# Optimization experiments

Hardware: AMD Instinct MI355X
Metric: run time of the kernel (lower is better)

## Reference

```python
import jax, jax.numpy as jnp
import numpy as np

N = 4096          # nodes in DAG
K = 14            # parents per non-root node
C = 1 << K        # CPT configurations per node
N_ROOTS = 64      # nodes with no parents
EPS = 1e-6


def setup_inputs() -> dict:
    key = jax.random.key(0)
    # CPT logits: original init is log(p/(1-p)) with p~U[0.1,0.9] -> roughly N(0,1)-scale
    logits = jax.random.normal(key, (N, C), dtype=jnp.float32)
    # DAG structure: node i >= N_ROOTS has K parents drawn from [0, i) => identity order is topological
    rng = np.random.default_rng(0)
    parents = np.zeros((N, K), dtype=np.int32)
    for i in range(N_ROOTS, N):
        parents[i] = rng.integers(0, i, size=K)
    root_mask = np.arange(N) < N_ROOTS
    # binary configuration matrix, MSB-first, same as _configs_matrix
    ints = np.arange(C)
    configs = ((ints[:, None] >> np.arange(K - 1, -1, -1)) & 1).astype(np.float32)  # [C, K]
    return {
        "logits": logits,
        "configs": jnp.asarray(configs),
        "parents": jnp.asarray(parents),
        "root_mask": jnp.asarray(root_mask),
    }


def reference(logits, configs, parents, root_mask):
    min_val = jnp.log(jnp.float32(EPS))
    max_val = jnp.log(jnp.float32(1.0 - EPS))

    def step(log_marg, xs):
        idx, logit_row, par, is_root = xs
        log_p_cpt = jax.nn.log_sigmoid(logit_row)                    # [C]
        plp = jnp.clip(log_marg[par], min_val, max_val)              # [K] parent log-marginals
        log1m = jnp.log1p(-jnp.minimum(jnp.exp(plp), 1.0 - EPS))     # [K] log(1 - p_parent)
        # sum_k configs*plp + (1-configs)*log1m == configs @ (plp - log1m) + sum(log1m)
        log_prod = configs @ (plp - log1m) + jnp.sum(log1m)          # [C]
        lm_nonroot = jax.nn.logsumexp(log_prod + log_p_cpt)
        lm = jnp.where(is_root, log_p_cpt[0], lm_nonroot)
        return log_marg.at[idx].set(lm), None

    n = logits.shape[0]
    init = jnp.zeros((n,), dtype=jnp.float32)
    xs = (jnp.arange(n), logits, parents, root_mask)
    log_marginals, _ = jax.lax.scan(step, init, xs)
    return jnp.exp(log_marginals)
```

## Files before the change

kernel.cpp:

```cpp
#include <hip/hip_runtime.h>
#include <math.h>
#include <stdint.h>


#define NN     4096
#define KK     14
#define CC     16384
#define NROOTS 64
#define NBLK   256
#define NTHR   1024
#define PT     (CC / NTHR)
#define SENTIN 0x7F7F7F7Fu

__global__ __launch_bounds__(NTHR, 4) void bayes_dag_kernel(
    const float* __restrict__ logits,
    const int*   __restrict__ parents,
    float*       __restrict__ out,
    unsigned*    __restrict__ flagv)
{
    __shared__ float pvals[KK];
    __shared__ float redLds[NTHR / 64];

    const int tid  = threadIdx.x;
    const int lane = tid & 63;
    const int wv   = tid >> 6;
    const float LOG2E = 1.4426950408889634f;

    int node = blockIdx.x;
    if (node < NROOTS) {
        if (tid == 0) {
            float x = logits[(size_t)node * CC];
            float p = __builtin_amdgcn_rcpf(1.f + exp2f(-x * LOG2E));
            out[node] = p;
            __hip_atomic_store(&flagv[node], __float_as_uint(p),
                               __ATOMIC_RELAXED, __HIP_MEMORY_SCOPE_AGENT);
        }
        node += NBLK;
    }

    float xs[PT];
    {
        const float* row = logits + (size_t)node * CC;
        #pragma unroll
        for (int m = 0; m < PT; ++m) xs[m] = row[m * NTHR + tid];
    }

    for (; node < NN; node += NBLK) {
        const int   nxt  = node + NBLK;
        const float* nrow = logits + (size_t)(nxt < NN ? nxt : node) * CC;
        float xn[PT];
        #pragma unroll
        for (int m = 0; m < PT; ++m) xn[m] = nrow[m * NTHR + tid];

        float sig[PT];
        #pragma unroll
        for (int m = 0; m < PT; ++m)
            sig[m] = __builtin_amdgcn_rcpf(1.f + exp2f(-xs[m] * LOG2E));

        if (wv == 0) {
            int p = 0;
            if (lane < KK) p = parents[node * KK + lane];
            unsigned v = SENTIN;
            int guard = 0;
            for (;;) {
                if (lane < KK)
                    v = __hip_atomic_load(&flagv[p], __ATOMIC_RELAXED,
                                          __HIP_MEMORY_SCOPE_AGENT);
                if (__all(lane >= KK || v != SENTIN)) break;
                if (++guard > (1 << 22)) break;
                __builtin_amdgcn_s_sleep(1);
            }
            if (lane < KK) {
                float pf = __uint_as_float(v);
                pvals[lane] = fminf(fmaxf(pf, 1e-6f), 1.f - 1e-6f);
            }
        }
        __syncthreads();

        float pv[KK];
        #pragma unroll
        for (int k = 0; k < KK; ++k) pv[k] = pvals[k];

        float v8[8];
        #pragma unroll
        for (int j = 0; j < 8; ++j)
            v8[j] = fmaf(pv[3], sig[2*j+1] - sig[2*j], sig[2*j]);
        float v4[4];
        #pragma unroll
        for (int j = 0; j < 4; ++j)
            v4[j] = fmaf(pv[2], v8[2*j+1] - v8[2*j], v8[2*j]);
        float v2[2];
        #pragma unroll
        for (int j = 0; j < 2; ++j)
            v2[j] = fmaf(pv[1], v4[2*j+1] - v4[2*j], v4[2*j]);
        float acc = fmaf(pv[0], v2[1] - v2[0], v2[0]);

        #pragma unroll
        for (int t = 0; t < 6; ++t) {
            float other = __shfl_xor(acc, 1 << t, 64);
            bool  bit   = (lane >> t) & 1;
            float a = bit ? other : acc;
            float b = bit ? acc : other;
            acc = fmaf(pv[13 - t], b - a, a);
        }
        if (lane == 0) redLds[wv] = acc;
        __syncthreads();

        if (wv == 0) {
            float val = (lane < NTHR / 64) ? redLds[lane] : 0.f;
            #pragma unroll
            for (int t = 0; t < 4; ++t) {
                float other = __shfl_xor(val, 1 << t, 64);
                bool  bit   = (lane >> t) & 1;
                float a = bit ? other : val;
                float b = bit ? val : other;
                val = fmaf(pv[7 - t], b - a, a);
            }
            if (lane == 0) {
                out[node] = val;
                __hip_atomic_store(&flagv[node], __float_as_uint(val),
                                   __ATOMIC_RELAXED, __HIP_MEMORY_SCOPE_AGENT);
            }
        }

        #pragma unroll
        for (int m = 0; m < PT; ++m) xs[m] = xn[m];
    }
}

extern "C" void kernel_launch(void* const* d_in, const int* in_sizes, int n_in,
                              void* d_out, int out_size, void* d_ws, size_t ws_size,
                              hipStream_t stream) {
    const float* logits  = (const float*)d_in[0];
    const int*   parents = (const int*)d_in[2];
    float*    out   = (float*)d_out;
    unsigned* flagv = (unsigned*)d_ws;

    hipMemsetAsync(flagv, 0x7F, NN * sizeof(unsigned), stream);

    void* args[] = { (void*)&logits, (void*)&parents, (void*)&out, (void*)&flagv };
    hipLaunchCooperativeKernel((const void*)bayes_dag_kernel,
                               dim3(NBLK), dim3(NTHR), args, 0, stream);
}
```

Measured before the change: 623.3 us.

## Start reduction with one missing parent and defer its fold to the end

The parent-wait loop now exits once all but one parent marginal is available. The block reduces the CPT tensor over every other parent, keeping two partial results split on the missing parent's bit, and waits for that last parent only just before the final fold. Next-node parent indices are prefetched, and the sleep in the poll loop is removed. This is meant to shorten the critical dependency chain across blocks, at the cost of more complex branching, duplicated shuffle reductions and busier polling.

```diff
diff --git a/kernel.cpp b/kernel.cpp
--- a/kernel.cpp
+++ b/kernel.cpp
@@ -12,6 +12,11 @@
 #define PT     (CC / NTHR)
 #define SENTIN 0x7F7F7F7Fu
 
+#define FOLD2(p, x0, x1) fmaf((p), (x1) - (x0), (x0))
+#define FOLD8(pA, pB, pC, s0,s1,s2,s3,s4,s5,s6,s7) \
+    FOLD2(pC, FOLD2(pB, FOLD2(pA, s0, s1), FOLD2(pA, s2, s3)), \
+              FOLD2(pB, FOLD2(pA, s4, s5), FOLD2(pA, s6, s7)))
+
 __global__ __launch_bounds__(NTHR, 4) void bayes_dag_kernel(
     const float* __restrict__ logits,
     const int*   __restrict__ parents,
@@ -19,7 +24,10 @@
     unsigned*    __restrict__ flagv)
 {
     __shared__ float pvals[KK];
-    __shared__ float redLds[NTHR / 64];
+    __shared__ int   sSlotLds;
+    __shared__ int   sParLds;
+    __shared__ float redA[NTHR / 64];
+    __shared__ float redB[NTHR / 64];
 
     const int tid  = threadIdx.x;
     const int lane = tid & 63;
@@ -31,9 +39,9 @@
         if (tid == 0) {
             float x = logits[(size_t)node * CC];
             float p = __builtin_amdgcn_rcpf(1.f + exp2f(-x * LOG2E));
-            out[node] = p;
             __hip_atomic_store(&flagv[node], __float_as_uint(p),
                                __ATOMIC_RELAXED, __HIP_MEMORY_SCOPE_AGENT);
+            out[node] = p;
         }
         node += NBLK;
     }
@@ -44,10 +52,14 @@
         #pragma unroll
         for (int m = 0; m < PT; ++m) xs[m] = row[m * NTHR + tid];
     }
+    int pcur = 0;
+    if (wv == 0 && lane < KK) pcur = parents[node * KK + lane];
 
     for (; node < NN; node += NBLK) {
-        const int   nxt  = node + NBLK;
-        const float* nrow = logits + (size_t)(nxt < NN ? nxt : node) * CC;
+        const int nxt    = node + NBLK;
+        const int nclamp = (nxt < NN) ? nxt : node;
+
+        const float* nrow = logits + (size_t)nclamp * CC;
         float xn[PT];
         #pragma unroll
         for (int m = 0; m < PT; ++m) xn[m] = nrow[m * NTHR + tid];
@@ -58,68 +70,136 @@
             sig[m] = __builtin_amdgcn_rcpf(1.f + exp2f(-xs[m] * LOG2E));
 
         if (wv == 0) {
-            int p = 0;
-            if (lane < KK) p = parents[node * KK + lane];
             unsigned v = SENTIN;
+            unsigned long long rdy;
             int guard = 0;
             for (;;) {
-                if (lane < KK)
-                    v = __hip_atomic_load(&flagv[p], __ATOMIC_RELAXED,
+                if (lane < KK && v == SENTIN)
+                    v = __hip_atomic_load(&flagv[pcur], __ATOMIC_RELAXED,
                                           __HIP_MEMORY_SCOPE_AGENT);
-                if (__all(lane >= KK || v != SENTIN)) break;
+                rdy = __ballot(lane >= KK || v != SENTIN);
+                if (__popcll(rdy) >= 63) break;
                 if (++guard > (1 << 22)) break;
-                __builtin_amdgcn_s_sleep(1);
-            }
+            }
+            unsigned long long miss = (~rdy) & 0x3FFFull;
+            int s  = miss ? __builtin_ctzll(miss) : -1;
+            int sp = __shfl(pcur, (s < 0) ? 0 : s, 64);
+            if (lane == 0) { sSlotLds = s; sParLds = sp; }
             if (lane < KK) {
                 float pf = __uint_as_float(v);
                 pvals[lane] = fminf(fmaxf(pf, 1e-6f), 1.f - 1e-6f);
             }
+            if (lane < KK) pcur = parents[nclamp * KK + lane];
         }
         __syncthreads();
 
+        const int s = sSlotLds;
         float pv[KK];
         #pragma unroll
         for (int k = 0; k < KK; ++k) pv[k] = pvals[k];
 
-        float v8[8];
-        #pragma unroll
-        for (int j = 0; j < 8; ++j)
-            v8[j] = fmaf(pv[3], sig[2*j+1] - sig[2*j], sig[2*j]);
-        float v4[4];
-        #pragma unroll
-        for (int j = 0; j < 4; ++j)
-            v4[j] = fmaf(pv[2], v8[2*j+1] - v8[2*j], v8[2*j]);
-        float v2[2];
-        #pragma unroll
-        for (int j = 0; j < 2; ++j)
-            v2[j] = fmaf(pv[1], v4[2*j+1] - v4[2*j], v4[2*j]);
-        float acc = fmaf(pv[0], v2[1] - v2[0], v2[0]);
-
+        float acc, acc1 = 0.f;
+        const bool regPair = (s >= 0 && s < 4);
+        switch (s) {
+            case 0:
+                acc  = FOLD8(pv[3],pv[2],pv[1], sig[0],sig[1],sig[2],sig[3],sig[4],sig[5],sig[6],sig[7]);
+                acc1 = FOLD8(pv[3],pv[2],pv[1], sig[8],sig[9],sig[10],sig[11],sig[12],sig[13],sig[14],sig[15]);
+                break;
+            case 1:
+                acc  = FOLD8(pv[3],pv[2],pv[0], sig[0],sig[1],sig[2],sig[3],sig[8],sig[9],sig[10],sig[11]);
+                acc1 = FOLD8(pv[3],pv[2],pv[0], sig[4],sig[5],sig[6],sig[7],sig[12],sig[13],sig[14],sig[15]);
+                break;
+            case 2:
+                acc  = FOLD8(pv[3],pv[1],pv[0], sig[0],sig[1],sig[4],sig[5],sig[8],sig[9],sig[12],sig[13]);
+                acc1 = FOLD8(pv[3],pv[1],pv[0], sig[2],sig[3],sig[6],sig[7],sig[10],sig[11],sig[14],sig[15]);
+                break;
+            case 3:
+                acc  = FOLD8(pv[2],pv[1],pv[0], sig[0],sig[2],sig[4],sig[6],sig[8],sig[10],sig[12],sig[14]);
+                acc1 = FOLD8(pv[2],pv[1],pv[0], sig[1],sig[3],sig[5],sig[7],sig[9],sig[11],sig[13],sig[15]);
+                break;
+            default:
+                acc = FOLD2(pv[0],
+                        FOLD8(pv[3],pv[2],pv[1], sig[0],sig[1],sig[2],sig[3],sig[4],sig[5],sig[6],sig[7]),
+                        FOLD8(pv[3],pv[2],pv[1], sig[8],sig[9],sig[10],sig[11],sig[12],sig[13],sig[14],sig[15]));
+                break;
+        }
+
+        const int st = (s >= 8) ? (13 - s) : -1;
         #pragma unroll
         for (int t = 0; t < 6; ++t) {
-            float other = __shfl_xor(acc, 1 << t, 64);
-            bool  bit   = (lane >> t) & 1;
-            float a = bit ? other : acc;
-            float b = bit ? acc : other;
-            acc = fmaf(pv[13 - t], b - a, a);
-        }
-        if (lane == 0) redLds[wv] = acc;
+            if (t == st) continue;
+            const float p = pv[13 - t];
+            {
+                float other = __shfl_xor(acc, 1 << t, 64);
+                bool  bit   = (lane >> t) & 1;
+                float a = bit ? other : acc;
+                float b = bit ? acc : other;
+                acc = fmaf(p, b - a, a);
+            }
+            if (regPair) {
+                float other = __shfl_xor(acc1, 1 << t, 64);
+                bool  bit   = (lane >> t) & 1;
+                float a = bit ? other : acc1;
+                float b = bit ? acc1 : other;
+                acc1 = fmaf(p, b - a, a);
+            }
+        }
+
+        if (regPair) {
+            if (lane == 0) { redA[wv] = acc; redB[wv] = acc1; }
+        } else if (st >= 0) {
+            if (lane == 0)         redA[wv] = acc;
+            if (lane == (1 << st)) redB[wv] = acc;
+        } else {
+            if (lane == 0) redA[wv] = acc;
+        }
         __syncthreads();
 
         if (wv == 0) {
-            float val = (lane < NTHR / 64) ? redLds[lane] : 0.f;
+            const bool pairAB = (s >= 0) && (s < 4 || s >= 8);
+            const int  tw     = (s >= 4 && s < 8) ? (7 - s) : -1;
+            float v0 = (lane < NTHR / 64) ? redA[lane] : 0.f;
+            float v1 = (pairAB && lane < NTHR / 64) ? redB[lane] : 0.f;
             #pragma unroll
             for (int t = 0; t < 4; ++t) {
-                float other = __shfl_xor(val, 1 << t, 64);
-                bool  bit   = (lane >> t) & 1;
-                float a = bit ? other : val;
-                float b = bit ? val : other;
-                val = fmaf(pv[7 - t], b - a, a);
+                if (t == tw) continue;
+                const float p = pv[7 - t];
+                {
+                    float other = __shfl_xor(v0, 1 << t, 64);
+                    bool  bit   = (lane >> t) & 1;
+                    float a = bit ? other : v0;
+                    float b = bit ? v0 : other;
+                    v0 = fmaf(p, b - a, a);
+                }
+                if (pairAB) {
+                    float other = __shfl_xor(v1, 1 << t, 64);
+                    bool  bit   = (lane >> t) & 1;
+                    float a = bit ? other : v1;
+                    float b = bit ? v1 : other;
+                    v1 = fmaf(p, b - a, a);
+                }
+            }
+            float res;
+            if (s < 0) {
+                res = v0;
+            } else {
+                float x0, x1;
+                if (tw >= 0) { x0 = __shfl(v0, 0, 64); x1 = __shfl(v0, 1 << tw, 64); }
+                else         { x0 = v0; x1 = v1; }
+                const int sp = sParLds;
+                unsigned u = __hip_atomic_load(&flagv[sp], __ATOMIC_RELAXED,
+                                               __HIP_MEMORY_SCOPE_AGENT);
+                int guard = 0;
+                while (u == SENTIN && ++guard < (1 << 23))
+                    u = __hip_atomic_load(&flagv[sp], __ATOMIC_RELAXED,
+                                          __HIP_MEMORY_SCOPE_AGENT);
+                float ps = fminf(fmaxf(__uint_as_float(u), 1e-6f), 1.f - 1e-6f);
+                res = fmaf(ps, x1 - x0, x0);
             }
             if (lane == 0) {
-                out[node] = val;
-                __hip_atomic_store(&flagv[node], __float_as_uint(val),
+                __hip_atomic_store(&flagv[node], __float_as_uint(res),
                                    __ATOMIC_RELAXED, __HIP_MEMORY_SCOPE_AGENT);
+                out[node] = res;
             }
         }
 
```

After: 521.0 us. 16.4% less time.

## Speculate on last missing parent by computing both branches, double grid size

Applied to the files above, without the earlier changes.

The parent-wait loop now proceeds once all but one parent marginal is available. For the missing parent it computes two folds, one with that parent fixed to 0 and one fixed to 1, and interpolates once the value arrives, taking the final parent wait off the critical path. The block size is halved to 512 threads and the grid raised to 512 blocks when occupancy allows, so each block covers fewer nodes. Parent indices and next-row loads are prefetched earlier. The cost is doubled fold arithmetic and extra registers, and the sleep in the spin loop is removed, which increases polling traffic.

```diff
diff --git a/kernel.cpp b/kernel.cpp
--- a/kernel.cpp
+++ b/kernel.cpp
@@ -7,10 +7,40 @@
 #define KK     14
 #define CC     16384
 #define NROOTS 64
-#define NBLK   256
-#define NTHR   1024
+#define NTHR   512
+#define NW     (NTHR / 64)
 #define PT     (CC / NTHR)
 #define SENTIN 0x7F7F7F7Fu
+
+#define FOLD2(p, x0, x1) fmaf((p), (x1) - (x0), (x0))
+
+#define LDFLAG(p) __hip_atomic_load(&flagv[(p)], __ATOMIC_RELAXED, \
+                                    __HIP_MEMORY_SCOPE_AGENT)
+
+#define DO_FOLD(P, SRC, OUTACC)                                         \
+    {                                                                   \
+        float t16[16];                                                  \
+        _Pragma("unroll") for (int i = 0; i < 16; ++i)                  \
+            t16[i] = FOLD2((P)[4], (SRC)[2*i], (SRC)[2*i+1]);           \
+        float t8[8];                                                    \
+        _Pragma("unroll") for (int i = 0; i < 8; ++i)                   \
+            t8[i] = FOLD2((P)[3], t16[2*i], t16[2*i+1]);                \
+        float t4[4];                                                    \
+        _Pragma("unroll") for (int i = 0; i < 4; ++i)                   \
+            t4[i] = FOLD2((P)[2], t8[2*i], t8[2*i+1]);                  \
+        float t2[2];                                                    \
+        _Pragma("unroll") for (int i = 0; i < 2; ++i)                   \
+            t2[i] = FOLD2((P)[1], t4[2*i], t4[2*i+1]);                  \
+        float a = FOLD2((P)[0], t2[0], t2[1]);                          \
+        _Pragma("unroll") for (int t = 0; t < 6; ++t) {                 \
+            float other = __shfl_xor(a, 1 << t, 64);                    \
+            bool  bit   = (lane >> t) & 1;                              \
+            float lo = bit ? other : a;                                 \
+            float hi = bit ? a : other;                                 \
+            a = fmaf((P)[13 - t], hi - lo, lo);                         \
+        }                                                               \
+        OUTACC = a;                                                     \
+    }
 
 __global__ __launch_bounds__(NTHR, 4) void bayes_dag_kernel(
     const float* __restrict__ logits,
@@ -19,11 +49,14 @@
     unsigned*    __restrict__ flagv)
 {
     __shared__ float pvals[KK];
-    __shared__ float redLds[NTHR / 64];
+    __shared__ int   sSlotLds;
+    __shared__ float redA[NW];
+    __shared__ float redB[NW];
 
-    const int tid  = threadIdx.x;
-    const int lane = tid & 63;
-    const int wv   = tid >> 6;
+    const int tid   = threadIdx.x;
+    const int lane  = tid & 63;
+    const int wv    = tid >> 6;
+    const int gstep = gridDim.x;
     const float LOG2E = 1.4426950408889634f;
 
     int node = blockIdx.x;
@@ -31,100 +64,111 @@
         if (tid == 0) {
             float x = logits[(size_t)node * CC];
             float p = __builtin_amdgcn_rcpf(1.f + exp2f(-x * LOG2E));
-            out[node] = p;
             __hip_atomic_store(&flagv[node], __float_as_uint(p),
                                __ATOMIC_RELAXED, __HIP_MEMORY_SCOPE_AGENT);
+            out[node] = p;
         }
-        node += NBLK;
+        node += gstep;
     }
 
-    float xs[PT];
+    float xn[PT];
     {
         const float* row = logits + (size_t)node * CC;
         #pragma unroll
-        for (int m = 0; m < PT; ++m) xs[m] = row[m * NTHR + tid];
+        for (int m = 0; m < PT; ++m) xn[m] = row[m * NTHR + tid];
     }
+    int pcur = 0;
+    if (wv == 0 && lane < KK) pcur = parents[node * KK + lane];
 
-    for (; node < NN; node += NBLK) {
-        const int   nxt  = node + NBLK;
-        const float* nrow = logits + (size_t)(nxt < NN ? nxt : node) * CC;
-        float xn[PT];
-        #pragma unroll
-        for (int m = 0; m < PT; ++m) xn[m] = nrow[m * NTHR + tid];
+    for (; node < NN; node += gstep) {
+        const int nxt    = node + gstep;
+        const int nclamp = (nxt < NN) ? nxt : node;
 
         float sig[PT];
         #pragma unroll
         for (int m = 0; m < PT; ++m)
-            sig[m] = __builtin_amdgcn_rcpf(1.f + exp2f(-xs[m] * LOG2E));
+            sig[m] = __builtin_amdgcn_rcpf(1.f + exp2f(-xn[m] * LOG2E));
 
+        const float* nrow = logits + (size_t)nclamp * CC;
+        #pragma unroll
+        for (int m = 0; m < PT; ++m) xn[m] = nrow[m * NTHR + tid];
+
+        int spLoc = 0;
         if (wv == 0) {
-            int p = 0;
-            if (lane < KK) p = parents[node * KK + lane];
             unsigned v = SENTIN;
+            unsigned long long rdy;
             int guard = 0;
             for (;;) {
-                if (lane < KK)
-                    v = __hip_atomic_load(&flagv[p], __ATOMIC_RELAXED,
-                                          __HIP_MEMORY_SCOPE_AGENT);
-                if (__all(lane >= KK || v != SENTIN)) break;
+                if (lane < KK && v == SENTIN)
+                    v = LDFLAG(pcur);
+                rdy = __ballot(lane >= KK || v != SENTIN);
+                if (__popcll(rdy) >= 63) break;
                 if (++guard > (1 << 22)) break;
-                __builtin_amdgcn_s_sleep(1);
             }
+            unsigned long long miss = (~rdy) & 0x3FFFull;
+            int s = miss ? __builtin_ctzll(miss) : -1;
+            spLoc = __shfl(pcur, (s < 0) ? 0 : s, 64);
+            if (lane == 0) sSlotLds = s;
             if (lane < KK) {
                 float pf = __uint_as_float(v);
                 pvals[lane] = fminf(fmaxf(pf, 1e-6f), 1.f - 1e-6f);
             }
+            if (lane < KK) pcur = parents[nclamp * KK + lane];
         }
         __syncthreads();
 
-        float pv[KK];
+        const int s = sSlotLds;
+        float pA[KK], pB[KK];
         #pragma unroll
-        for (int k = 0; k < KK; ++k) pv[k] = pvals[k];
+        for (int k = 0; k < KK; ++k) {
+            float v = pvals[k];
+            pA[k] = (k == s) ? 0.f : v;
+            pB[k] = (k == s) ? 1.f : v;
+        }
 
-        float v8[8];
-        #pragma unroll
-        for (int j = 0; j < 8; ++j)
-            v8[j] = fmaf(pv[3], sig[2*j+1] - sig[2*j], sig[2*j]);
-        float v4[4];
-        #pragma unroll
-        for (int j = 0; j < 4; ++j)
-            v4[j] = fmaf(pv[2], v8[2*j+1] - v8[2*j], v8[2*j]);
-        float v2[2];
-        #pragma unroll
-        for (int j = 0; j < 2; ++j)
-            v2[j] = fmaf(pv[1], v4[2*j+1] - v4[2*j], v4[2*j]);
-        float acc = fmaf(pv[0], v2[1] - v2[0], v2[0]);
-
-        #pragma unroll
-        for (int t = 0; t < 6; ++t) {
-            float other = __shfl_xor(acc, 1 << t, 64);
-            bool  bit   = (lane >> t) & 1;
-            float a = bit ? other : acc;
-            float b = bit ? acc : other;
-            acc = fmaf(pv[13 - t], b - a, a);
-        }
-        if (lane == 0) redLds[wv] = acc;
+        float accA, accB;
+        DO_FOLD(pA, sig, accA);
+        DO_FOLD(pB, sig, accB);
+        if (lane == 0) { redA[wv] = accA; redB[wv] = accB; }
         __syncthreads();
 
         if (wv == 0) {
-            float val = (lane < NTHR / 64) ? redLds[lane] : 0.f;
+            float vA = (lane < NW) ? redA[lane] : 0.f;
+            float vB = (lane < NW) ? redB[lane] : 0.f;
             #pragma unroll
-            for (int t = 0; t < 4; ++t) {
-                float other = __shfl_xor(val, 1 << t, 64);
-                bool  bit   = (lane >> t) & 1;
-                float a = bit ? other : val;
-                float b = bit ? val : other;
-                val = fmaf(pv[7 - t], b - a, a);
+            for (int t = 0; t < 3; ++t) {
+                {
+                    float other = __shfl_xor(vA, 1 << t, 64);
+                    bool  bit   = (lane >> t) & 1;
+                    float lo = bit ? other : vA;
+                    float hi = bit ? vA : other;
+                    vA = fmaf(pA[7 - t], hi - lo, lo);
+                }
+                {
+                    float other = __shfl_xor(vB, 1 << t, 64);
+                    bool  bit   = (lane >> t) & 1;
+                    float lo = bit ? other : vB;
+                    float hi = bit ? vB : other;
+                    vB = fmaf(pB[7 - t], hi - lo, lo);
+                }
+            }
+            float res;
+            if (s < 0) {
+                res = vA;
+            } else {
+                unsigned u = LDFLAG(spLoc);
+                int guard = 0;
+                while (u == SENTIN && ++guard < (1 << 23))
+                    u = LDFLAG(spLoc);
+                float ps = fminf(fmaxf(__uint_as_float(u), 1e-6f), 1.f - 1e-6f);
+                res = fmaf(ps, vB - vA, vA);
             }
             if (lane == 0) {
-                out[node] = val;
-                __hip_atomic_store(&flagv[node], __float_as_uint(val),
+                __hip_atomic_store(&flagv[node], __float_as_uint(res),
                                    __ATOMIC_RELAXED, __HIP_MEMORY_SCOPE_AGENT);
+                out[node] = res;
             }
         }
-
-        #pragma unroll
-        for (int m = 0; m < PT; ++m) xs[m] = xn[m];
     }
 }
 
@@ -136,9 +180,17 @@
     float*    out   = (float*)d_out;
     unsigned* flagv = (unsigned*)d_ws;
 
+    static int grid = 0;
+    if (grid == 0) {
+        int maxb = 0;
+        hipError_t e = hipOccupancyMaxActiveBlocksPerMultiprocessor(
+            &maxb, (const void*)bayes_dag_kernel, NTHR, 0);
+        grid = (e == hipSuccess && maxb >= 2) ? 512 : 256;
+    }
+
     hipMemsetAsync(flagv, 0x7F, NN * sizeof(unsigned), stream);
 
     void* args[] = { (void*)&logits, (void*)&parents, (void*)&out, (void*)&flagv };
     hipLaunchCooperativeKernel((const void*)bayes_dag_kernel,
-                               dim3(NBLK), dim3(NTHR), args, 0, stream);
+                               dim3(grid), dim3(NTHR), args, 0, stream);
 }
```

Result: faster. 551.0 us (-11.6%).
